# Performance work log

Hardware: AMD Instinct MI355X
Metric: run time of the kernel (lower is better)

The kernel has to match this reference:

```python
import jax, jax.numpy as jnp
import numpy as np

N = 100000
E = 1600000

def _build_adj(edge_index):
    # add self-loops (set_diag), then symmetric DAD normalization
    loops = jnp.arange(N, dtype=edge_index.dtype)
    row = jnp.concatenate([edge_index[0], loops])
    col = jnp.concatenate([edge_index[1], loops])
    deg = jax.ops.segment_sum(jnp.ones_like(row, dtype=jnp.float32), row, num_segments=N)
    dinv = jnp.where(deg > 0, jax.lax.rsqrt(deg), 0.0)
    norm = dinv[row] * dinv[col]  # [E+N]
    return row, col, norm

def _spmm(row, col, norm, h):
    # out[row] += norm * h[col]  (A_hat @ h)
    return jax.ops.segment_sum(norm[:, None] * h[col], row, num_segments=N)

def setup_inputs() -> dict:
    key = jax.random.key(0)
    ks = jax.random.split(key, 8)
    nfeat, nhid, nclass = 128, 128, 64
    s = lambda d: (1.0 / np.sqrt(d)).astype(np.float32)
    return {
        "x": jax.random.normal(ks[0], (N, nfeat), jnp.float32),
        "edge_index": jax.random.randint(ks[1], (2, E), 0, N, dtype=jnp.int64),
        "W0": jax.random.normal(ks[2], (nfeat, nhid), jnp.float32) * s(nfeat),
        "b0": jnp.zeros((nhid,), jnp.float32),
        "W1": jax.random.normal(ks[3], (nhid, nhid), jnp.float32) * s(nhid),
        "b1": jnp.zeros((nhid,), jnp.float32),
        "W2": jax.random.normal(ks[4], (nhid, nclass), jnp.float32) * s(nhid),
        "b2": jnp.zeros((nclass,), jnp.float32),
    }

def reference(x, edge_index, W0, b0, W1, b1, W2, b2):
    row, col, norm = _build_adj(edge_index)
    # layer 1: GCNConv + relu (dropout inactive in eval mode)
    h = jax.nn.relu(_spmm(row, col, norm, x @ W0) + b0)
    # layer 2
    h = jax.nn.relu(_spmm(row, col, norm, h @ W1) + b1)
    # final layer, no activation
    return _spmm(row, col, norm, h @ W2) + b2
```

## Files before the change

kernel.cpp:

```cpp
#include <hip/hip_runtime.h>
#include <hip/hip_bf16.h>

#define NN 100000
#define NE 1600000
#define BK 98
#define CAP 18432
#define CHUNK 8192

typedef _Float16 f16;
typedef f16 f16x8 __attribute__((ext_vector_type(8)));
typedef float f32x4 __attribute__((ext_vector_type(4)));


__global__ __launch_bounds__(256) void bin_edges(const int* __restrict__ row,
                                                 const int* __restrict__ col,
                                                 int* __restrict__ bcursor,
                                                 int2* __restrict__ binned) {
    __shared__ int  bcnt[BK];
    __shared__ int  bbase[BK];
    __shared__ int  lstart[BK + 1];
    __shared__ int  bcur[BK];
    __shared__ int2 stage[CHUNK];
    int tid = threadIdx.x;
    int e0 = blockIdx.x * CHUNK;
    int emax = min(CHUNK, NE - e0);

    if (tid < BK) bcnt[tid] = 0;
    __syncthreads();
    for (int i = tid; i < emax; i += 256)
        atomicAdd(&bcnt[row[e0 + i] >> 10], 1);
    __syncthreads();
    if (tid == 0) {
        int s = 0;
        for (int b = 0; b < BK; ++b) { lstart[b] = s; s += bcnt[b]; }
        lstart[BK] = s;
    }
    __syncthreads();
    if (tid < BK) {
        bcur[tid]  = lstart[tid];
        bbase[tid] = atomicAdd(&bcursor[tid], bcnt[tid]);
    }
    __syncthreads();
    for (int i = tid; i < emax; i += 256) {
        int r = row[e0 + i], c = col[e0 + i];
        int pos = atomicAdd(&bcur[r >> 10], 1);
        stage[pos] = make_int2(r, c);
    }
    __syncthreads();
    for (int i = tid; i < emax; i += 256) {
        int2 rc = stage[i];
        int b = rc.x >> 10;
        binned[(size_t)b * CAP + bbase[b] + (i - lstart[b])] = rc;
    }
}

__global__ __launch_bounds__(1024) void build_csr(const int* __restrict__ bcount,
                                                  const int2* __restrict__ binned,
                                                  int* __restrict__ offsets,
                                                  float* __restrict__ dinv,
                                                  int* __restrict__ csr_col) {
    __shared__ int cnt[1024];
    __shared__ int sc[1024];
    __shared__ int colbuf[CAP];
    __shared__ int mybase_s;
    int tid = threadIdx.x;
    int b = blockIdx.x;
    int r0 = b << 10;
    int nrows = min(1024, NN - r0);

    if (tid < BK) sc[tid] = bcount[tid];
    cnt[tid] = 0;
    __syncthreads();
    if (tid == 0) {
        int s = 0;
        for (int i = 0; i < b; ++i) s += sc[i];
        mybase_s = s;
    }
    int n = sc[b];
    __syncthreads();
    int mybase = mybase_s;
    const int2* src = binned + (size_t)b * CAP;

    for (int i = tid; i < n; i += 1024)
        atomicAdd(&cnt[src[i].x - r0], 1);
    __syncthreads();

    int v = cnt[tid];
    sc[tid] = v;
    __syncthreads();
    #pragma unroll
    for (int s = 1; s < 1024; s <<= 1) {
        int t = (tid >= s) ? sc[tid - s] : 0;
        __syncthreads();
        sc[tid] += t;
        __syncthreads();
    }
    int incl = sc[tid];
    if (tid < nrows) {
        offsets[r0 + tid + 1] = mybase + incl;
        dinv[r0 + tid] = rsqrtf((float)(v + 1));
    }
    if (b == 0 && tid == 0) offsets[0] = 0;

    cnt[tid] = incl - v;
    __syncthreads();
    for (int i = tid; i < n; i += 1024) {
        int2 rc = src[i];
        int pos = atomicAdd(&cnt[rc.x - r0], 1);
        colbuf[pos] = rc.y;
    }
    __syncthreads();
    for (int i = tid; i < n; i += 1024)
        csr_col[mybase + i] = colbuf[i];
}

template<int F, bool AFP32>
__global__ __launch_bounds__(256) void gemm_mfma(const void* __restrict__ Ain,
                                                 const float* __restrict__ W,
                                                 const float* __restrict__ dinv,
                                                 f16* __restrict__ T) {
    constexpr int PITCH = 136;
    __shared__ f16 Wt[F * PITCH];
    int tid = threadIdx.x;
    for (int e = tid; e < 128 * F; e += 256) {
        int k = e / F, n = e - k * F;
        Wt[n * PITCH + k] = (f16)W[e];
    }
    __syncthreads();

    int wave = tid >> 6;
    int lane = tid & 63;
    int m = lane & 15, q = lane >> 4;
    int r0 = blockIdx.x * 64 + wave * 16;
    int ra = min(r0 + m, NN - 1);

    constexpr int NT = F / 16;
    f32x4 acc[NT];
    #pragma unroll
    for (int t = 0; t < NT; ++t) acc[t] = (f32x4){0.f, 0.f, 0.f, 0.f};

    #pragma unroll
    for (int c = 0; c < 4; ++c) {
        f16x8 a;
        if constexpr (AFP32) {
            const float* Af = (const float*)Ain;
            const float4* p = (const float4*)&Af[(size_t)ra * 128 + c * 32 + q * 8];
            float4 lo = p[0], hi = p[1];
            a[0] = (f16)lo.x; a[1] = (f16)lo.y; a[2] = (f16)lo.z; a[3] = (f16)lo.w;
            a[4] = (f16)hi.x; a[5] = (f16)hi.y; a[6] = (f16)hi.z; a[7] = (f16)hi.w;
        } else {
            const f16* Ah = (const f16*)Ain;
            a = *(const f16x8*)&Ah[(size_t)ra * 128 + c * 32 + q * 8];
        }
        #pragma unroll
        for (int t = 0; t < NT; ++t) {
            f16x8 b = *(const f16x8*)&Wt[(t * 16 + m) * PITCH + c * 32 + q * 8];
            acc[t] = __builtin_amdgcn_mfma_f32_16x16x32_f16(a, b, acc[t], 0, 0, 0);
        }
    }

    int rows[4];
    float dv[4];
    #pragma unroll
    for (int i = 0; i < 4; ++i) {
        rows[i] = r0 + q * 4 + i;
        dv[i] = dinv[min(rows[i], NN - 1)];
    }
    #pragma unroll
    for (int t = 0; t < NT; ++t) {
        #pragma unroll
        for (int i = 0; i < 4; ++i) {
            if (rows[i] < NN) {
                T[(size_t)rows[i] * F + t * 16 + m] = (f16)(acc[t][i] * dv[i]);
            }
        }
    }
}

template<int F2>
__global__ __launch_bounds__(512, 6) void spmm_gemm(const f16* __restrict__ T,
                                                    const int* __restrict__ offsets,
                                                    const int* __restrict__ csr_col,
                                                    const float* __restrict__ dinv,
                                                    const float* __restrict__ bias,
                                                    const float* __restrict__ W,
                                                    f16* __restrict__ Tout) {
    constexpr int PITCH = 136;
    __shared__ f16 Wt[F2 * PITCH];
    __shared__ f16 hbuf[32 * PITCH];
    int tid = threadIdx.x;

    for (int e = tid; e < 128 * F2; e += 512) {
        int k = e / F2, n = e - k * F2;
        Wt[n * PITCH + k] = (f16)W[e];
    }

    int lane = tid & 15;
    int rs   = tid >> 4;
    int r    = blockIdx.x * 32 + rs;

    const f16x8* Tv = (const f16x8*)T;
    int o0 = offsets[r], o1 = offsets[r + 1];

    float s0[8], s1[8], s2[8], s3[8];
    f16x8 self = Tv[(size_t)r * 16 + lane];
    #pragma unroll
    for (int u = 0; u < 8; ++u) { s0[u] = (float)self[u]; s1[u] = 0.f; s2[u] = 0.f; s3[u] = 0.f; }

    int j = o0;
    for (; j + 4 <= o1; j += 4) {
        int c0 = csr_col[j], c1 = csr_col[j + 1], c2 = csr_col[j + 2], c3 = csr_col[j + 3];
        f16x8 v0 = Tv[(size_t)c0 * 16 + lane];
        f16x8 v1 = Tv[(size_t)c1 * 16 + lane];
        f16x8 v2 = Tv[(size_t)c2 * 16 + lane];
        f16x8 v3 = Tv[(size_t)c3 * 16 + lane];
        #pragma unroll
        for (int u = 0; u < 8; ++u) {
            s0[u] += (float)v0[u]; s1[u] += (float)v1[u];
            s2[u] += (float)v2[u]; s3[u] += (float)v3[u];
        }
    }
    for (; j < o1; ++j) {
        int c = csr_col[j];
        f16x8 v = Tv[(size_t)c * 16 + lane];
        #pragma unroll
        for (int u = 0; u < 8; ++u) s0[u] += (float)v[u];
    }

    float dr = dinv[r];
    f16x8 h;
    #pragma unroll
    for (int u = 0; u < 8; ++u) {
        float s = (s0[u] + s1[u]) + (s2[u] + s3[u]);
        float o = fmaf(dr, s, bias[lane * 8 + u]);
        h[u] = (f16)fmaxf(o, 0.f);
    }
    *(f16x8*)&hbuf[rs * PITCH + lane * 8] = h;
    __syncthreads();

    int wv = tid >> 6, wl = tid & 63;
    int m = wl & 15, q = wl >> 4;
    constexpr int FW  = F2 / 4;
    constexpr int NTW = FW / 16;
    int rg = wv >> 2;
    int fg = wv & 3;

    f32x4 acc[NTW];
    #pragma unroll
    for (int t = 0; t < NTW; ++t) acc[t] = (f32x4){0.f, 0.f, 0.f, 0.f};

    #pragma unroll
    for (int c = 0; c < 4; ++c) {
        f16x8 a = *(const f16x8*)&hbuf[(rg * 16 + m) * PITCH + c * 32 + q * 8];
        #pragma unroll
        for (int t = 0; t < NTW; ++t) {
            f16x8 b = *(const f16x8*)&Wt[(fg * FW + t * 16 + m) * PITCH + c * 32 + q * 8];
            acc[t] = __builtin_amdgcn_mfma_f32_16x16x32_f16(a, b, acc[t], 0, 0, 0);
        }
    }
    __syncthreads();

    #pragma unroll
    for (int i = 0; i < 4; ++i) {
        int rloc = rg * 16 + q * 4 + i;
        float dv = dinv[blockIdx.x * 32 + rloc];
        #pragma unroll
        for (int t = 0; t < NTW; ++t)
            hbuf[rloc * PITCH + fg * FW + t * 16 + m] = (f16)(acc[t][i] * dv);
    }
    __syncthreads();

    constexpr int LPO = F2 / 8;
    for (int e = tid; e < 32 * LPO; e += 512) {
        int rr = e / LPO, ff = e - rr * LPO;
        ((f16x8*)Tout)[(size_t)(blockIdx.x * 32 + rr) * LPO + ff] =
            *(f16x8*)&hbuf[rr * PITCH + ff * 8];
    }
}

template<int F, bool RELU, bool OUTF16>
__global__ __launch_bounds__(256) void spmm_h(const f16* __restrict__ T,
                                              const int* __restrict__ offsets,
                                              const int* __restrict__ csr_col,
                                              const float* __restrict__ dinv,
                                              const float* __restrict__ bias,
                                              void* __restrict__ outv) {
    constexpr int LPR = F / 8;
    constexpr int RPB = 256 / LPR;
    int lane = threadIdx.x % LPR;
    int rs   = threadIdx.x / LPR;
    int r    = blockIdx.x * RPB + rs;
    if (r >= NN) return;

    const f16x8* Tv = (const f16x8*)T;
    int o0 = offsets[r], o1 = offsets[r + 1];

    float s0[8], s1[8], s2[8], s3[8];
    f16x8 self = Tv[(size_t)r * LPR + lane];
    #pragma unroll
    for (int u = 0; u < 8; ++u) { s0[u] = (float)self[u]; s1[u] = 0.f; s2[u] = 0.f; s3[u] = 0.f; }

    int j = o0;
    for (; j + 4 <= o1; j += 4) {
        int c0 = csr_col[j], c1 = csr_col[j + 1], c2 = csr_col[j + 2], c3 = csr_col[j + 3];
        f16x8 v0 = Tv[(size_t)c0 * LPR + lane];
        f16x8 v1 = Tv[(size_t)c1 * LPR + lane];
        f16x8 v2 = Tv[(size_t)c2 * LPR + lane];
        f16x8 v3 = Tv[(size_t)c3 * LPR + lane];
        #pragma unroll
        for (int u = 0; u < 8; ++u) {
            s0[u] += (float)v0[u]; s1[u] += (float)v1[u];
            s2[u] += (float)v2[u]; s3[u] += (float)v3[u];
        }
    }
    for (; j < o1; ++j) {
        int c = csr_col[j];
        f16x8 v = Tv[(size_t)c * LPR + lane];
        #pragma unroll
        for (int u = 0; u < 8; ++u) s0[u] += (float)v[u];
    }

    float dr = dinv[r];
    float o[8];
    #pragma unroll
    for (int u = 0; u < 8; ++u) {
        float s = (s0[u] + s1[u]) + (s2[u] + s3[u]);
        o[u] = fmaf(dr, s, bias[lane * 8 + u]);
        if (RELU) o[u] = fmaxf(o[u], 0.f);
    }

    if (OUTF16) {
        f16x8 h;
        #pragma unroll
        for (int u = 0; u < 8; ++u) h[u] = (f16)o[u];
        ((f16x8*)outv)[(size_t)r * LPR + lane] = h;
    } else {
        float* outF = (float*)outv;
        float4 lo = make_float4(o[0], o[1], o[2], o[3]);
        float4 hi = make_float4(o[4], o[5], o[6], o[7]);
        *(float4*)&outF[(size_t)r * F + lane * 8]     = lo;
        *(float4*)&outF[(size_t)r * F + lane * 8 + 4] = hi;
    }
}


extern "C" void kernel_launch(void* const* d_in, const int* in_sizes, int n_in,
                              void* d_out, int out_size, void* d_ws, size_t ws_size,
                              hipStream_t stream) {
    const float* x  = (const float*)d_in[0];
    const int*   ei = (const int*)d_in[1];
    const float* W0 = (const float*)d_in[2];
    const float* b0 = (const float*)d_in[3];
    const float* W1 = (const float*)d_in[4];
    const float* b1 = (const float*)d_in[5];
    const float* W2 = (const float*)d_in[6];
    const float* b2 = (const float*)d_in[7];
    float* out = (float*)d_out;

    const int* row = ei;
    const int* col = ei + NE;

    char* wsp = (char*)d_ws;
    auto alloc = [&](size_t bytes) {
        char* p = wsp;
        wsp += (bytes + 255) & ~(size_t)255;
        return p;
    };
    int*   bcursor = (int*)alloc((size_t)BK * 4);
    int2*  binned  = (int2*)alloc((size_t)BK * CAP * 8);
    int*   offsets = (int*)alloc((size_t)(NN + 1) * 4);
    float* dinv    = (float*)alloc((size_t)NN * 4);
    int*   csr_col = (int*)alloc((size_t)NE * 4);
    f16*   Tbuf    = (f16*)alloc((size_t)NN * 128 * 2);
    f16*   Hbuf    = (f16*)alloc((size_t)NN * 128 * 2);

    hipMemsetAsync(bcursor, 0, (size_t)BK * 4, stream);
    bin_edges<<<(NE + CHUNK - 1) / CHUNK, 256, 0, stream>>>(row, col, bcursor, binned);
    build_csr<<<BK, 1024, 0, stream>>>(bcursor, binned, offsets, dinv, csr_col);

    const int GB = (NN + 63) / 64;
    const int FB = NN / 32;

    gemm_mfma<128, true><<<GB, 256, 0, stream>>>(x, W0, dinv, Tbuf);
    spmm_gemm<128><<<FB, 512, 0, stream>>>(Tbuf, offsets, csr_col, dinv, b0, W1, Hbuf);
    spmm_gemm<64><<<FB, 512, 0, stream>>>(Hbuf, offsets, csr_col, dinv, b1, W2, Tbuf);
    spmm_h<64, false, false><<<(NN + 31) / 32, 256, 0, stream>>>(Tbuf, offsets, csr_col, dinv, b2, out);
}
```

Before: 346.4 us.

## Use finer 256-row bins for CSR build and unroll gathers by eight

Edge binning now uses 391 buckets of 256 rows instead of 98 buckets of 1024 rows. Each bin_edges block handles a smaller chunk and computes its bucket prefix sum with a parallel scan instead of a serial loop. build_csr now runs 391 blocks of 256 threads, which fills more compute units, and computes its base offset with a tree reduction. The SpMM gather loops are unrolled by eight, with more loads in flight, and fold into two accumulators instead of four. The risk is a bin overflowing its CAP2 capacity if degrees are skewed, and a longer dependency chain in the accumulators.

```diff
diff --git a/kernel.cpp b/kernel.cpp
--- a/kernel.cpp
+++ b/kernel.cpp
@@ -3,9 +3,9 @@
 
 #define NN 100000
 #define NE 1600000
-#define BK 98
-#define CAP 18432
-#define CHUNK 8192
+#define BK2 391
+#define CAP2 4864
+#define CHUNK2 4096
 
 typedef _Float16 f16;
 typedef f16 f16x8 __attribute__((ext_vector_type(8)));
@@ -16,72 +16,82 @@
                                                  const int* __restrict__ col,
                                                  int* __restrict__ bcursor,
                                                  int2* __restrict__ binned) {
-    __shared__ int  bcnt[BK];
-    __shared__ int  bbase[BK];
-    __shared__ int  lstart[BK + 1];
-    __shared__ int  bcur[BK];
-    __shared__ int2 stage[CHUNK];
+    __shared__ int  bcnt[BK2];
+    __shared__ int  bbase[BK2];
+    __shared__ int  lstart[BK2];
+    __shared__ int  bcur[BK2];
+    __shared__ int  sca[BK2];
+    __shared__ int  scb[BK2];
+    __shared__ int2 stage[CHUNK2];
     int tid = threadIdx.x;
-    int e0 = blockIdx.x * CHUNK;
-    int emax = min(CHUNK, NE - e0);
-
-    if (tid < BK) bcnt[tid] = 0;
+    int e0 = blockIdx.x * CHUNK2;
+    int emax = min(CHUNK2, NE - e0);
+
+    for (int i = tid; i < BK2; i += 256) bcnt[i] = 0;
     __syncthreads();
     for (int i = tid; i < emax; i += 256)
-        atomicAdd(&bcnt[row[e0 + i] >> 10], 1);
-    __syncthreads();
-    if (tid == 0) {
-        int s = 0;
-        for (int b = 0; b < BK; ++b) { lstart[b] = s; s += bcnt[b]; }
-        lstart[BK] = s;
-    }
-    __syncthreads();
-    if (tid < BK) {
-        bcur[tid]  = lstart[tid];
-        bbase[tid] = atomicAdd(&bcursor[tid], bcnt[tid]);
-    }
-    __syncthreads();
+        atomicAdd(&bcnt[row[e0 + i] >> 8], 1);
+    __syncthreads();
+
+    for (int i = tid; i < BK2; i += 256) sca[i] = bcnt[i];
+    __syncthreads();
+    int* pa = sca; int* pb = scb;
+    for (int s = 1; s < BK2; s <<= 1) {
+        for (int i = tid; i < BK2; i += 256)
+            pb[i] = pa[i] + ((i >= s) ? pa[i - s] : 0);
+        __syncthreads();
+        int* t = pa; pa = pb; pb = t;
+    }
+    for (int i = tid; i < BK2; i += 256) {
+        int ex = pa[i] - bcnt[i];
+        lstart[i] = ex;
+        bcur[i]   = ex;
+        bbase[i]  = atomicAdd(&bcursor[i], bcnt[i]);
+    }
+    __syncthreads();
+
     for (int i = tid; i < emax; i += 256) {
         int r = row[e0 + i], c = col[e0 + i];
-        int pos = atomicAdd(&bcur[r >> 10], 1);
+        int pos = atomicAdd(&bcur[r >> 8], 1);
         stage[pos] = make_int2(r, c);
     }
     __syncthreads();
     for (int i = tid; i < emax; i += 256) {
         int2 rc = stage[i];
-        int b = rc.x >> 10;
-        binned[(size_t)b * CAP + bbase[b] + (i - lstart[b])] = rc;
-    }
-}
-
-__global__ __launch_bounds__(1024) void build_csr(const int* __restrict__ bcount,
-                                                  const int2* __restrict__ binned,
-                                                  int* __restrict__ offsets,
-                                                  float* __restrict__ dinv,
-                                                  int* __restrict__ csr_col) {
-    __shared__ int cnt[1024];
-    __shared__ int sc[1024];
-    __shared__ int colbuf[CAP];
-    __shared__ int mybase_s;
+        int b = rc.x >> 8;
+        binned[(size_t)b * CAP2 + bbase[b] + (i - lstart[b])] = rc;
+    }
+}
+
+__global__ __launch_bounds__(256) void build_csr(const int* __restrict__ bcount,
+                                                 const int2* __restrict__ binned,
+                                                 int* __restrict__ offsets,
+                                                 float* __restrict__ dinv,
+                                                 int* __restrict__ csr_col) {
+    __shared__ int cnt[256];
+    __shared__ int sc[256];
+    __shared__ int red[256];
+    __shared__ int colbuf[CAP2];
     int tid = threadIdx.x;
     int b = blockIdx.x;
-    int r0 = b << 10;
-    int nrows = min(1024, NN - r0);
-
-    if (tid < BK) sc[tid] = bcount[tid];
+    int r0 = b << 8;
+    int nrows = min(256, NN - r0);
+
+    int part = 0;
+    for (int i = tid; i < b; i += 256) part += bcount[i];
+    red[tid] = part;
     cnt[tid] = 0;
     __syncthreads();
-    if (tid == 0) {
-        int s = 0;
-        for (int i = 0; i < b; ++i) s += sc[i];
-        mybase_s = s;
-    }
-    int n = sc[b];
-    __syncthreads();
-    int mybase = mybase_s;
-    const int2* src = binned + (size_t)b * CAP;
-
-    for (int i = tid; i < n; i += 1024)
+    #pragma unroll
+    for (int s = 128; s > 0; s >>= 1) {
+        if (tid < s) red[tid] += red[tid + s];
+        __syncthreads();
+    }
+    int mybase = red[0];
+    int n = bcount[b];
+    const int2* src = binned + (size_t)b * CAP2;
+
+    for (int i = tid; i < n; i += 256)
         atomicAdd(&cnt[src[i].x - r0], 1);
     __syncthreads();
 
@@ -89,7 +99,7 @@
     sc[tid] = v;
     __syncthreads();
     #pragma unroll
-    for (int s = 1; s < 1024; s <<= 1) {
+    for (int s = 1; s < 256; s <<= 1) {
         int t = (tid >= s) ? sc[tid - s] : 0;
         __syncthreads();
         sc[tid] += t;
@@ -104,13 +114,13 @@
 
     cnt[tid] = incl - v;
     __syncthreads();
-    for (int i = tid; i < n; i += 1024) {
+    for (int i = tid; i < n; i += 256) {
         int2 rc = src[i];
         int pos = atomicAdd(&cnt[rc.x - r0], 1);
         colbuf[pos] = rc.y;
     }
     __syncthreads();
-    for (int i = tid; i < n; i += 1024)
+    for (int i = tid; i < n; i += 256)
         csr_col[mybase + i] = colbuf[i];
 }
 
@@ -202,12 +212,31 @@
     const f16x8* Tv = (const f16x8*)T;
     int o0 = offsets[r], o1 = offsets[r + 1];
 
-    float s0[8], s1[8], s2[8], s3[8];
+    float s0[8], s1[8];
     f16x8 self = Tv[(size_t)r * 16 + lane];
     #pragma unroll
-    for (int u = 0; u < 8; ++u) { s0[u] = (float)self[u]; s1[u] = 0.f; s2[u] = 0.f; s3[u] = 0.f; }
+    for (int u = 0; u < 8; ++u) { s0[u] = (float)self[u]; s1[u] = 0.f; }
 
     int j = o0;
+    for (; j + 8 <= o1; j += 8) {
+        int c0 = csr_col[j],     c1 = csr_col[j + 1], c2 = csr_col[j + 2], c3 = csr_col[j + 3];
+        int c4 = csr_col[j + 4], c5 = csr_col[j + 5], c6 = csr_col[j + 6], c7 = csr_col[j + 7];
+        f16x8 v0 = Tv[(size_t)c0 * 16 + lane];
+        f16x8 v1 = Tv[(size_t)c1 * 16 + lane];
+        f16x8 v2 = Tv[(size_t)c2 * 16 + lane];
+        f16x8 v3 = Tv[(size_t)c3 * 16 + lane];
+        f16x8 v4 = Tv[(size_t)c4 * 16 + lane];
+        f16x8 v5 = Tv[(size_t)c5 * 16 + lane];
+        f16x8 v6 = Tv[(size_t)c6 * 16 + lane];
+        f16x8 v7 = Tv[(size_t)c7 * 16 + lane];
+        #pragma unroll
+        for (int u = 0; u < 8; ++u) {
+            s0[u] += (float)v0[u] + (float)v2[u];
+            s1[u] += (float)v1[u] + (float)v3[u];
+            s0[u] += (float)v4[u] + (float)v6[u];
+            s1[u] += (float)v5[u] + (float)v7[u];
+        }
+    }
     for (; j + 4 <= o1; j += 4) {
         int c0 = csr_col[j], c1 = csr_col[j + 1], c2 = csr_col[j + 2], c3 = csr_col[j + 3];
         f16x8 v0 = Tv[(size_t)c0 * 16 + lane];
@@ -216,8 +245,8 @@
         f16x8 v3 = Tv[(size_t)c3 * 16 + lane];
         #pragma unroll
         for (int u = 0; u < 8; ++u) {
-            s0[u] += (float)v0[u]; s1[u] += (float)v1[u];
-            s2[u] += (float)v2[u]; s3[u] += (float)v3[u];
+            s0[u] += (float)v0[u] + (float)v2[u];
+            s1[u] += (float)v1[u] + (float)v3[u];
         }
     }
     for (; j < o1; ++j) {
@@ -231,7 +260,7 @@
     f16x8 h;
     #pragma unroll
     for (int u = 0; u < 8; ++u) {
-        float s = (s0[u] + s1[u]) + (s2[u] + s3[u]);
+        float s = s0[u] + s1[u];
         float o = fmaf(dr, s, bias[lane * 8 + u]);
         h[u] = (f16)fmaxf(o, 0.f);
     }
@@ -295,12 +324,31 @@
     const f16x8* Tv = (const f16x8*)T;
     int o0 = offsets[r], o1 = offsets[r + 1];
 
-    float s0[8], s1[8], s2[8], s3[8];
+    float s0[8], s1[8];
     f16x8 self = Tv[(size_t)r * LPR + lane];
     #pragma unroll
-    for (int u = 0; u < 8; ++u) { s0[u] = (float)self[u]; s1[u] = 0.f; s2[u] = 0.f; s3[u] = 0.f; }
+    for (int u = 0; u < 8; ++u) { s0[u] = (float)self[u]; s1[u] = 0.f; }
 
     int j = o0;
+    for (; j + 8 <= o1; j += 8) {
+        int c0 = csr_col[j],     c1 = csr_col[j + 1], c2 = csr_col[j + 2], c3 = csr_col[j + 3];
+        int c4 = csr_col[j + 4], c5 = csr_col[j + 5], c6 = csr_col[j + 6], c7 = csr_col[j + 7];
+        f16x8 v0 = Tv[(size_t)c0 * LPR + lane];
+        f16x8 v1 = Tv[(size_t)c1 * LPR + lane];
+        f16x8 v2 = Tv[(size_t)c2 * LPR + lane];
+        f16x8 v3 = Tv[(size_t)c3 * LPR + lane];
+        f16x8 v4 = Tv[(size_t)c4 * LPR + lane];
+        f16x8 v5 = Tv[(size_t)c5 * LPR + lane];
+        f16x8 v6 = Tv[(size_t)c6 * LPR + lane];
+        f16x8 v7 = Tv[(size_t)c7 * LPR + lane];
+        #pragma unroll
+        for (int u = 0; u < 8; ++u) {
+            s0[u] += (float)v0[u] + (float)v2[u];
+            s1[u] += (float)v1[u] + (float)v3[u];
+            s0[u] += (float)v4[u] + (float)v6[u];
+            s1[u] += (float)v5[u] + (float)v7[u];
+        }
+    }
     for (; j + 4 <= o1; j += 4) {
         int c0 = csr_col[j], c1 = csr_col[j + 1], c2 = csr_col[j + 2], c3 = csr_col[j + 3];
         f16x8 v0 = Tv[(size_t)c0 * LPR + lane];
@@ -309,8 +357,8 @@
         f16x8 v3 = Tv[(size_t)c3 * LPR + lane];
         #pragma unroll
         for (int u = 0; u < 8; ++u) {
-            s0[u] += (float)v0[u]; s1[u] += (float)v1[u];
-            s2[u] += (float)v2[u]; s3[u] += (float)v3[u];
+            s0[u] += (float)v0[u] + (float)v2[u];
+            s1[u] += (float)v1[u] + (float)v3[u];
         }
     }
     for (; j < o1; ++j) {
@@ -324,7 +372,7 @@
     float o[8];
     #pragma unroll
     for (int u = 0; u < 8; ++u) {
-        float s = (s0[u] + s1[u]) + (s2[u] + s3[u]);
+        float s = s0[u] + s1[u];
         o[u] = fmaf(dr, s, bias[lane * 8 + u]);
         if (RELU) o[u] = fmaxf(o[u], 0.f);
     }
@@ -366,17 +414,17 @@
         wsp += (bytes + 255) & ~(size_t)255;
         return p;
     };
-    int*   bcursor = (int*)alloc((size_t)BK * 4);
-    int2*  binned  = (int2*)alloc((size_t)BK * CAP * 8);
+    int*   bcursor = (int*)alloc((size_t)BK2 * 4);
+    int2*  binned  = (int2*)alloc((size_t)BK2 * CAP2 * 8);
     int*   offsets = (int*)alloc((size_t)(NN + 1) * 4);
     float* dinv    = (float*)alloc((size_t)NN * 4);
     int*   csr_col = (int*)alloc((size_t)NE * 4);
     f16*   Tbuf    = (f16*)alloc((size_t)NN * 128 * 2);
     f16*   Hbuf    = (f16*)alloc((size_t)NN * 128 * 2);
 
-    hipMemsetAsync(bcursor, 0, (size_t)BK * 4, stream);
-    bin_edges<<<(NE + CHUNK - 1) / CHUNK, 256, 0, stream>>>(row, col, bcursor, binned);
-    build_csr<<<BK, 1024, 0, stream>>>(bcursor, binned, offsets, dinv, csr_col);
+    hipMemsetAsync(bcursor, 0, (size_t)BK2 * 4, stream);
+    bin_edges<<<(NE + CHUNK2 - 1) / CHUNK2, 256, 0, stream>>>(row, col, bcursor, binned);
+    build_csr<<<BK2, 256, 0, stream>>>(bcursor, binned, offsets, dinv, csr_col);
 
     const int GB = (NN + 63) / 64;
     const int FB = NN / 32;
```

New measurement: 335.1 us. 3.2% less time.
